# Optimization experiments

Hardware: AMD Instinct MI355X
Metric: run time of the kernel (lower is better)

Reference implementation:

```python
import jax, jax.numpy as jnp
import numpy as np

K = 16  # hardcoded in the torch module (reshape([-1, 16]))


def setup_inputs() -> dict:
    key = jax.random.key(0)
    B, M = 32, 2048
    N = B * M
    ks = jax.random.split(key, 7)
    pos = jax.random.normal(ks[0], (N, 3), dtype=jnp.float32)
    batch = jnp.repeat(jnp.arange(B, dtype=jnp.int32), M)  # sorted, equal-size graphs

    def lin(k_, fi, fo):
        lim = 1.0 / np.sqrt(fi)
        w = jax.random.uniform(k_, (fi, fo), jnp.float32, -lim, lim)
        b = jax.random.uniform(jax.random.fold_in(k_, 1), (fo,), jnp.float32, -lim, lim)
        return w, b

    W1, b1 = lin(ks[1], K * 6, 1024)
    W2, b2 = lin(ks[2], 1024, 256)
    W3, b3 = lin(ks[3], 256, 9)
    return {"pos": pos, "batch": batch, "num_graphs": B,
            "W1": W1, "b1": b1, "W2": W2, "b2": b2, "W3": W3, "b3": b3}


def _knn_idx(pos, num_graphs):
    # equal-size graphs laid out contiguously -> batched brute-force knn
    N = pos.shape[0]
    M = N // num_graphs
    p = pos.reshape(num_graphs, M, 3)
    sq = jnp.sum(p * p, axis=-1)                      # [B, M]
    # squared distances [B, M, M]; self-distance ~0 so loop=True self-edge is kept
    d2 = sq[:, :, None] + sq[:, None, :] - 2.0 * jnp.einsum('bid,bjd->bij', p, p)
    _, idx = jax.lax.top_k(-d2, K)                    # [B, M, K] local indices
    offs = (jnp.arange(num_graphs, dtype=idx.dtype) * M)[:, None, None]
    return (idx + offs).reshape(N, K)                 # global neighbour indices


def reference(pos, batch, num_graphs, W1, b1, W2, b2, W3, b3):
    N = pos.shape[0]
    M = N // num_graphs
    nbr_idx = _knn_idx(pos, num_graphs)               # [N, K]
    neighbours = pos[nbr_idx]                         # [N, K, 3] gather
    center = pos[:, None, :]                          # [N, 1, 3]
    feat = jnp.concatenate(
        [jnp.broadcast_to(center, (N, K, 3)), center - neighbours], axis=2
    ).reshape(N, K * 6)                               # [N, 96]
    h = jax.nn.relu(feat @ W1 + b1)
    h = jax.nn.relu(h @ W2 + b2)
    x9 = h @ W3 + b3                                  # [N, 9]
    pooled = x9.reshape(num_graphs, M, 9).mean(axis=1)  # global_mean_pool -> [B, 9]
    T = pooled[batch].reshape(N, 3, 3)                # gather back per node
    return jnp.einsum('nd,ndk->nk', pos, T)           # bmm([N,1,3],[N,3,3]) squeezed
```

## Files before the change

kernel.cpp:

```cpp
#include <hip/hip_runtime.h>
#include <stdint.h>

#define NPTS   65536
#define MPTS   2048
#define NGRAPH 32

typedef short s16x8 __attribute__((ext_vector_type(8)));
typedef float f32x4 __attribute__((ext_vector_type(4)));

#define FEATP_OFF 0u
#define W1P_OFF   12582912u
#define W2P_OFF   12779520u
#define SACC_OFF  13303808u
#define POOLT_OFF 13336576u

__device__ __forceinline__ unsigned short f2bf(float f) {
  unsigned u = __float_as_uint(f);
  u = (u + 0x7FFFu + ((u >> 16) & 1u)) >> 16;
  return (unsigned short)u;
}

__device__ __forceinline__ void ce32(unsigned& a, unsigned& b) {
  unsigned lo = __builtin_elementwise_min(a, b);
  b = __builtin_elementwise_max(a, b);
  a = lo;
}

template <int N>
__device__ __forceinline__ void sortN(unsigned* k) {
#pragma unroll
  for (int p = 1; p < N; p <<= 1)
#pragma unroll
    for (int q = p; q >= 1; q >>= 1)
#pragma unroll
      for (int j = q % p; j + q < N; j += 2 * q)
#pragma unroll
        for (int i = 0; i < q; ++i)
          if (i + j + q < N)
            if ((i + j) / (2 * p) == (i + j + q) / (2 * p))
              ce32(k[i + j], k[i + j + q]);
}

__device__ __forceinline__ void mergelow8(unsigned r[8], const unsigned b[8]) {
#pragma unroll
  for (int i = 0; i < 8; ++i)
    r[i] = __builtin_elementwise_min(r[i], b[7 - i]);
#pragma unroll
  for (int d = 4; d >= 1; d >>= 1)
#pragma unroll
    for (int i = 0; i < 8; ++i)
      if ((i & d) == 0) ce32(r[i], r[i + d]);
}

__device__ __forceinline__ void mergelow16(unsigned r[16], const unsigned b[16]) {
#pragma unroll
  for (int i = 0; i < 16; ++i)
    r[i] = __builtin_elementwise_min(r[i], b[15 - i]);
#pragma unroll
  for (int d = 8; d >= 1; d >>= 1)
#pragma unroll
    for (int i = 0; i < 16; ++i)
      if ((i & d) == 0) ce32(r[i], r[i + d]);
}

__global__ __launch_bounds__(256) void pack_w(
    const float* __restrict__ W1, const float* __restrict__ W2,
    unsigned short* __restrict__ w1p, unsigned short* __restrict__ w2p,
    float* __restrict__ sacc)
{
  int tid = blockIdx.x * 256 + threadIdx.x;
  if (tid < 96 * 1024) {
    int k = tid >> 10, n = tid & 1023;
    int kt = k >> 5, h = (k >> 3) & 3, j = k & 7;
    int nt = n >> 4, cc = n & 15;
    w1p[((size_t)(kt * 64 + nt) * 64 + h * 16 + cc) * 8 + j] = f2bf(W1[tid]);
  } else if (tid < 98304 + 262144) {
    int t = tid - 98304;
    int k = t >> 8, n = t & 255;
    int kt = k >> 5, h = (k >> 3) & 3, j = k & 7;
    int nt = n >> 4, cc = n & 15;
    w2p[((size_t)(kt * 16 + nt) * 64 + h * 16 + cc) * 8 + j] = f2bf(W2[t]);
  } else if (tid < 360448 + 8192) {
    sacc[tid - 360448] = 0.0f;
  }
}

__global__ __launch_bounds__(512, 4) void knn_feat(
    const float* __restrict__ pos, unsigned short* __restrict__ featp)
{
  __shared__ float4 pts[MPTS];
  int g = blockIdx.x >> 5;
  const float* gp = pos + (size_t)g * MPTS * 3;
  for (int i = threadIdx.x; i < MPTS; i += 512) {
    float x = gp[i * 3], y = gp[i * 3 + 1], z = gp[i * 3 + 2];
    float sq = fmaf(x, x, fmaf(y, y, z * z));
    pts[(i >> 8) + ((i & 255) << 3)] = make_float4(x, y, z, sq);
  }
  __syncthreads();

  int l = threadIdx.x & 63, w = threadIdx.x >> 6;
  int s = l >> 3, qlocal = l & 7;
  int ql = ((blockIdx.x & 31) << 6) + w * 8 + qlocal;
  float4 c = pts[(ql >> 8) + ((ql & 255) << 3)];
  float cs = c.w;
  unsigned sbase = (unsigned)(s << 8);

  unsigned run[8];

  {
    unsigned k[16];
#pragma unroll
    for (int t = 0; t < 16; ++t) {
      float4 p = pts[s + (t << 3)];
      float dot = fmaf(c.x, p.x, fmaf(c.y, p.y, c.z * p.z));
      float d2 = fmaf(-2.0f, dot, cs + p.w);
      k[t] = (__float_as_uint(d2) & 0xFFFFF800u) | sbase | (unsigned)t;
    }
    sortN<8>(k); sortN<8>(k + 8);
    mergelow8(k, k + 8);
#pragma unroll
    for (int i = 0; i < 8; ++i) run[i] = k[i];
  }
  for (int ch = 1; ch < 16; ++ch) {
    unsigned bch = sbase | (unsigned)(ch * 16);
    unsigned k[16];
#pragma unroll
    for (int t = 0; t < 16; ++t) {
      int i = ch * 16 + t;
      float4 p = pts[s + (i << 3)];
      float dot = fmaf(c.x, p.x, fmaf(c.y, p.y, c.z * p.z));
      float d2 = fmaf(-2.0f, dot, cs + p.w);
      k[t] = (__float_as_uint(d2) & 0xFFFFF800u) | bch | (unsigned)t;
    }
    sortN<8>(k); sortN<8>(k + 8);
    mergelow8(k, k + 8);
    mergelow8(run, k);
  }

  unsigned t16[16];
  {
    unsigned oth[8];
#pragma unroll
    for (int i = 0; i < 8; ++i) oth[i] = __shfl_xor(run[i], 8, 64);
#pragma unroll
    for (int i = 0; i < 8; ++i) {
      unsigned a = run[i], x = oth[7 - i];
      t16[i]     = __builtin_elementwise_min(a, x);
      t16[i + 8] = __builtin_elementwise_max(a, x);
    }
#pragma unroll
    for (int d = 4; d >= 1; d >>= 1)
#pragma unroll
      for (int i = 0; i < 16; ++i)
        if ((i & d) == 0) ce32(t16[i], t16[i + d]);
  }
#pragma unroll
  for (int m = 16; m <= 32; m <<= 1) {
    unsigned o2[16];
#pragma unroll
    for (int i = 0; i < 16; ++i) o2[i] = __shfl_xor(t16[i], m, 64);
    mergelow16(t16, o2);
  }

  if (s == 0) {
    float nx[16], ny[16], nz[16];
#pragma unroll
    for (int i = 0; i < 16; ++i) {
      int j = (int)(t16[i] & 0x7ffu);
      float4 p = pts[(j >> 8) + ((j & 255) << 3)];
      nx[i] = p.x; ny[i] = p.y; nz[i] = p.z;
    }
    int n = g * MPTS + ql;
    unsigned short* op = featp + (size_t)(n >> 4) * 1536 + (size_t)(n & 15) * 8;
#pragma unroll
    for (int kt = 0; kt < 3; ++kt) {
#pragma unroll
      for (int h = 0; h < 4; ++h) {
        s16x8 v;
#pragma unroll
        for (int j = 0; j < 8; ++j) {
          int f = kt * 32 + h * 8 + j;
          int kn = f / 6, comp = f % 6;
          float val;
          if      (comp == 0) val = c.x;
          else if (comp == 1) val = c.y;
          else if (comp == 2) val = c.z;
          else if (comp == 3) val = c.x - nx[kn];
          else if (comp == 4) val = c.y - ny[kn];
          else                val = c.z - nz[kn];
          v[j] = (short)f2bf(val);
        }
        *(s16x8*)(op + kt * 512 + h * 128) = v;
      }
    }
  }
}

__global__ __launch_bounds__(512, 2) void mlp_fused(
    const unsigned short* __restrict__ featp,
    const unsigned short* __restrict__ w1p,
    const unsigned short* __restrict__ w2p,
    const float* __restrict__ b1, const float* __restrict__ b2,
    float* __restrict__ sacc)
{
  __shared__ unsigned short h1c[2][64][136];

  int tid = threadIdx.x;
  int w = tid >> 6, lane = tid & 63;
  int b = blockIdx.x;
  int g = b >> 5;
  int ks = lane >> 4;
  int cl = lane & 15;

  s16x8 a1[4][3];
#pragma unroll
  for (int m = 0; m < 4; ++m) {
    const unsigned short* ap = featp + (size_t)(b * 4 + m) * 1536 + (size_t)lane * 8;
#pragma unroll
    for (int kt = 0; kt < 3; ++kt) a1[m][kt] = *(const s16x8*)(ap + kt * 512);
  }

  f32x4 acc2[4][2];
#pragma unroll
  for (int m = 0; m < 4; ++m) {
    acc2[m][0] = (f32x4){0, 0, 0, 0};
    acc2[m][1] = (f32x4){0, 0, 0, 0};
  }

  s16x8 b1f[3];
#pragma unroll
  for (int kt = 0; kt < 3; ++kt)
    b1f[kt] = *(const s16x8*)(w1p + ((size_t)(kt * 64 + w) * 64 + lane) * 8);

  for (int c = 0; c < 8; ++c) {
    int buf = c & 1;
    s16x8 b2f[8];
#pragma unroll
    for (int kt2 = 0; kt2 < 4; ++kt2)
#pragma unroll
      for (int j = 0; j < 2; ++j)
        b2f[kt2 * 2 + j] = *(const s16x8*)(
            w2p + ((size_t)((c * 4 + kt2) * 16 + (w * 2 + j)) * 64 + lane) * 8);

    float bias1 = b1[(c * 8 + w) * 16 + cl];
#pragma unroll
    for (int m = 0; m < 4; ++m) {
      f32x4 acc1 = (f32x4){0, 0, 0, 0};
#pragma unroll
      for (int kt = 0; kt < 3; ++kt)
        acc1 = __builtin_amdgcn_mfma_f32_16x16x32_bf16(a1[m][kt], b1f[kt], acc1, 0, 0, 0);
#pragma unroll
      for (int r = 0; r < 4; ++r) {
        float v = acc1[r] + bias1;
        v = v > 0.0f ? v : 0.0f;
        h1c[buf][m * 16 + ks * 4 + r][w * 16 + cl] = f2bf(v);
      }
    }

    if (c < 7) {
#pragma unroll
      for (int kt = 0; kt < 3; ++kt)
        b1f[kt] = *(const s16x8*)(
            w1p + ((size_t)(kt * 64 + (c + 1) * 8 + w) * 64 + lane) * 8);
    }
    __syncthreads();

#pragma unroll
    for (int kt2 = 0; kt2 < 4; ++kt2) {
      s16x8 afr[4];
#pragma unroll
      for (int m = 0; m < 4; ++m)
        afr[m] = *(const s16x8*)&h1c[buf][m * 16 + cl][kt2 * 32 + ks * 8];
#pragma unroll
      for (int j = 0; j < 2; ++j)
#pragma unroll
        for (int m = 0; m < 4; ++m)
          acc2[m][j] = __builtin_amdgcn_mfma_f32_16x16x32_bf16(
              afr[m], b2f[kt2 * 2 + j], acc2[m][j], 0, 0, 0);
    }
  }

  float sj0 = 0.0f, sj1 = 0.0f;
  {
    float bias20 = b2[(2 * w + 0) * 16 + cl];
    float bias21 = b2[(2 * w + 1) * 16 + cl];
#pragma unroll
    for (int m = 0; m < 4; ++m)
#pragma unroll
      for (int r = 0; r < 4; ++r) {
        float v0 = acc2[m][0][r] + bias20;
        float v1 = acc2[m][1][r] + bias21;
        sj0 += v0 > 0.0f ? v0 : 0.0f;
        sj1 += v1 > 0.0f ? v1 : 0.0f;
      }
  }
#pragma unroll
  for (int m = 16; m <= 32; m <<= 1) {
    sj0 += __shfl_xor(sj0, m, 64);
    sj1 += __shfl_xor(sj1, m, 64);
  }
  if (ks == 0) {
    atomicAdd(&sacc[g * 256 + (2 * w + 0) * 16 + cl], sj0);
    atomicAdd(&sacc[g * 256 + (2 * w + 1) * 16 + cl], sj1);
  }
}

__global__ __launch_bounds__(96) void pool_w3(
    const float* __restrict__ sacc, const float* __restrict__ W3,
    const float* __restrict__ b3, float* __restrict__ pooledT)
{
  int gid = blockIdx.x * 96 + threadIdx.x;
  if (gid >= NGRAPH * 9) return;
  int g = gid / 9, o = gid % 9;
  float acc = 0.0f;
  const float* sp = sacc + g * 256;
#pragma unroll 8
  for (int k = 0; k < 256; ++k) acc = fmaf(sp[k], W3[k * 9 + o], acc);
  pooledT[gid] = fmaf(acc, 1.0f / (float)MPTS, b3[o]);
}

__global__ __launch_bounds__(256) void finalize(
    const float* __restrict__ pos, const int* __restrict__ batch,
    const float* __restrict__ pooledT, float* __restrict__ out)
{
  int n = blockIdx.x * 256 + threadIdx.x;
  if (n >= NPTS) return;
  int bb = batch[n];
  float px = pos[n * 3], py = pos[n * 3 + 1], pz = pos[n * 3 + 2];
  const float* P = pooledT + bb * 9;
#pragma unroll
  for (int k2 = 0; k2 < 3; ++k2)
    out[n * 3 + k2] = fmaf(px, P[k2], fmaf(py, P[3 + k2], pz * P[6 + k2]));
}

extern "C" void kernel_launch(void* const* d_in, const int* in_sizes, int n_in,
                              void* d_out, int out_size, void* d_ws, size_t ws_size,
                              hipStream_t stream) {
  const float* pos  = (const float*)d_in[0];
  const int*   batch = (const int*)d_in[1];
  const float* W1 = (const float*)d_in[3];
  const float* b1 = (const float*)d_in[4];
  const float* W2 = (const float*)d_in[5];
  const float* b2 = (const float*)d_in[6];
  const float* W3 = (const float*)d_in[7];
  const float* b3 = (const float*)d_in[8];

  char* ws = (char*)d_ws;
  unsigned short* featp = (unsigned short*)(ws + FEATP_OFF);
  unsigned short* w1p   = (unsigned short*)(ws + W1P_OFF);
  unsigned short* w2p   = (unsigned short*)(ws + W2P_OFF);
  float*          sacc  = (float*)(ws + SACC_OFF);
  float*          pooledT = (float*)(ws + POOLT_OFF);
  float*          out = (float*)d_out;

  pack_w<<<dim3(1440), dim3(256), 0, stream>>>(W1, W2, w1p, w2p, sacc);
  knn_feat<<<dim3(1024), dim3(512), 0, stream>>>(pos, featp);
  mlp_fused<<<dim3(1024), dim3(512), 0, stream>>>(featp, w1p, w2p, b1, b2, sacc);
  pool_w3<<<dim3(3), dim3(96), 0, stream>>>(sacc, W3, b3, pooledT);
  finalize<<<dim3(256), dim3(256), 0, stream>>>(pos, batch, pooledT, out);
}
```

Measured before the change: 122.5 us.

## Replace brute-force kNN with z-sorted window search and early termination

Adds a per-graph bitonic sort of points by z-coordinate in the prep kernel, merged with the weight-packing kernel. The kNN kernel then walks outward from each query's rank in z order in 64-point chunks and stops once the z-gap squared exceeds the current 16th-best distance. This avoids scanning all 2048 candidates per query. It adds a sort pass and data-dependent, wave-divergent loop counts; with Gaussian data the pruning in 1D may be weak, and the threshold uses truncated keys, so there is some risk around ties and exactness.

Result: slower. 170.4 us (+39.1%).

```diff
diff --git a/kernel.cpp b/kernel.cpp
--- a/kernel.cpp
+++ b/kernel.cpp
@@ -13,6 +13,7 @@
 #define W2P_OFF   12779520u
 #define SACC_OFF  13303808u
 #define POOLT_OFF 13336576u
+#define ZKEY_OFF  13337728u
 
 __device__ __forceinline__ unsigned short f2bf(float f) {
   unsigned u = __float_as_uint(f);
@@ -63,85 +64,123 @@
       if ((i & d) == 0) ce32(r[i], r[i + d]);
 }
 
-__global__ __launch_bounds__(256) void pack_w(
-    const float* __restrict__ W1, const float* __restrict__ W2,
+__global__ __launch_bounds__(512) void prep(
+    const float* __restrict__ pos, const float* __restrict__ W1,
+    const float* __restrict__ W2, unsigned* __restrict__ zkeysG,
     unsigned short* __restrict__ w1p, unsigned short* __restrict__ w2p,
     float* __restrict__ sacc)
 {
-  int tid = blockIdx.x * 256 + threadIdx.x;
-  if (tid < 96 * 1024) {
-    int k = tid >> 10, n = tid & 1023;
-    int kt = k >> 5, h = (k >> 3) & 3, j = k & 7;
-    int nt = n >> 4, cc = n & 15;
-    w1p[((size_t)(kt * 64 + nt) * 64 + h * 16 + cc) * 8 + j] = f2bf(W1[tid]);
-  } else if (tid < 98304 + 262144) {
-    int t = tid - 98304;
-    int k = t >> 8, n = t & 255;
-    int kt = k >> 5, h = (k >> 3) & 3, j = k & 7;
-    int nt = n >> 4, cc = n & 15;
-    w2p[((size_t)(kt * 16 + nt) * 64 + h * 16 + cc) * 8 + j] = f2bf(W2[t]);
-  } else if (tid < 360448 + 8192) {
-    sacc[tid - 360448] = 0.0f;
+  __shared__ unsigned sk[MPTS];
+  int b = blockIdx.x;
+  if (b < NGRAPH) {
+    const float* gp = pos + (size_t)b * MPTS * 3;
+#pragma unroll
+    for (int e = 0; e < 4; ++e) {
+      int i = threadIdx.x + (e << 9);
+      float z = gp[i * 3 + 2];
+      unsigned u = __float_as_uint(z);
+      u ^= ((unsigned)(((int)u) >> 31)) | 0x80000000u;
+      sk[i] = (u & 0xFFFFF800u) | (unsigned)i;
+    }
+    for (int k2 = 2; k2 <= MPTS; k2 <<= 1)
+      for (int j = k2 >> 1; j > 0; j >>= 1) {
+        __syncthreads();
+#pragma unroll
+        for (int e = 0; e < 4; ++e) {
+          int i = threadIdx.x + (e << 9);
+          int ix = i ^ j;
+          if (ix > i) {
+            unsigned a = sk[i], bb = sk[ix];
+            bool up = ((i & k2) == 0);
+            if ((a > bb) == up) { sk[i] = bb; sk[ix] = a; }
+          }
+        }
+      }
+    __syncthreads();
+#pragma unroll
+    for (int e = 0; e < 4; ++e) {
+      int i = threadIdx.x + (e << 9);
+      zkeysG[(b << 11) + i] = sk[i];
+    }
+  } else {
+    int pid = (b - NGRAPH) * 512 + threadIdx.x;
+    if (pid < 98304) {
+      int k = pid >> 10, n = pid & 1023;
+      int kt = k >> 5, h = (k >> 3) & 3, j = k & 7;
+      int nt = n >> 4, cc = n & 15;
+      w1p[((size_t)(kt * 64 + nt) * 64 + h * 16 + cc) * 8 + j] = f2bf(W1[pid]);
+    } else if (pid < 98304 + 262144) {
+      int t = pid - 98304;
+      int k = t >> 8, n = t & 255;
+      int kt = k >> 5, h = (k >> 3) & 3, j = k & 7;
+      int nt = n >> 4, cc = n & 15;
+      w2p[((size_t)(kt * 16 + nt) * 64 + h * 16 + cc) * 8 + j] = f2bf(W2[t]);
+    } else if (pid < 360448 + 8192) {
+      sacc[pid - 360448] = 0.0f;
+    }
   }
 }
 
 __global__ __launch_bounds__(512, 4) void knn_feat(
-    const float* __restrict__ pos, unsigned short* __restrict__ featp)
+    const float* __restrict__ pos, const unsigned* __restrict__ zkeysG,
+    unsigned short* __restrict__ featp)
 {
-  __shared__ float4 pts[MPTS];
+  __shared__ float4 zpts[MPTS];
   int g = blockIdx.x >> 5;
   const float* gp = pos + (size_t)g * MPTS * 3;
   for (int i = threadIdx.x; i < MPTS; i += 512) {
-    float x = gp[i * 3], y = gp[i * 3 + 1], z = gp[i * 3 + 2];
-    float sq = fmaf(x, x, fmaf(y, y, z * z));
-    pts[(i >> 8) + ((i & 255) << 3)] = make_float4(x, y, z, sq);
+    int o = (int)(zkeysG[(g << 11) + i] & 0x7FFu);
+    float x = gp[o * 3], y = gp[o * 3 + 1], z = gp[o * 3 + 2];
+    zpts[i] = make_float4(x, y, z, fmaf(x, x, fmaf(y, y, z * z)));
   }
   __syncthreads();
 
   int l = threadIdx.x & 63, w = threadIdx.x >> 6;
-  int s = l >> 3, qlocal = l & 7;
-  int ql = ((blockIdx.x & 31) << 6) + w * 8 + qlocal;
-  float4 c = pts[(ql >> 8) + ((ql & 255) << 3)];
-  float cs = c.w;
-  unsigned sbase = (unsigned)(s << 8);
+  int t = l & 7, qv = l >> 3;
+  int R = ((blockIdx.x & 31) << 6) + w * 8 + qv;
+  float4 c = zpts[R];
+  float cs = c.w, cz = c.z;
 
   unsigned run[8];
-
-  {
-    unsigned k[16];
-#pragma unroll
-    for (int t = 0; t < 16; ++t) {
-      float4 p = pts[s + (t << 3)];
-      float dot = fmaf(c.x, p.x, fmaf(c.y, p.y, c.z * p.z));
-      float d2 = fmaf(-2.0f, dot, cs + p.w);
-      k[t] = (__float_as_uint(d2) & 0xFFFFF800u) | sbase | (unsigned)t;
-    }
-    sortN<8>(k); sortN<8>(k + 8);
-    mergelow8(k, k + 8);
-#pragma unroll
-    for (int i = 0; i < 8; ++i) run[i] = k[i];
-  }
-  for (int ch = 1; ch < 16; ++ch) {
-    unsigned bch = sbase | (unsigned)(ch * 16);
-    unsigned k[16];
-#pragma unroll
-    for (int t = 0; t < 16; ++t) {
-      int i = ch * 16 + t;
-      float4 p = pts[s + (i << 3)];
-      float dot = fmaf(c.x, p.x, fmaf(c.y, p.y, c.z * p.z));
-      float d2 = fmaf(-2.0f, dot, cs + p.w);
-      k[t] = (__float_as_uint(d2) & 0xFFFFF800u) | bch | (unsigned)t;
-    }
-    sortN<8>(k); sortN<8>(k + 8);
-    mergelow8(k, k + 8);
+#pragma unroll
+  for (int i = 0; i < 8; ++i) run[i] = 0xFFFFFFFFu;
+
+  int LO = R, HI = R;
+  for (int step = 0; step < 34; ++step) {
+    float dzl = (LO > 0)    ? (cz - zpts[LO - 1].z) : 1e30f;
+    float dzr = (HI < MPTS) ? (zpts[HI].z - cz)     : 1e30f;
+    bool goR = dzr <= dzl;
+    int base = goR ? HI : LO - 64;
+    if (goR) HI += 64; else LO -= 64;
+
+    unsigned k[8];
+#pragma unroll
+    for (int kk = 0; kk < 8; ++kk) {
+      int p = base + t + (kk << 3);
+      int pc = min(max(p, 0), MPTS - 1);
+      float4 P = zpts[pc];
+      float dot = fmaf(c.x, P.x, fmaf(c.y, P.y, c.z * P.z));
+      float d2 = fmaf(-2.0f, dot, cs + P.w);
+      unsigned key = (__float_as_uint(d2) & 0xFFFFF800u) | (unsigned)pc;
+      k[kk] = ((unsigned)p < (unsigned)MPTS) ? key : 0xFFFFFFFFu;
+    }
+    sortN<8>(k);
     mergelow8(run, k);
+
+    unsigned t0 = run[7] | 0x7FFu;
+    unsigned thr = (t0 > 0xFFFEFFFFu) ? 0xFFFFFFFFu : t0 + 0x10000u;
+    float dl = (LO > 0)    ? (cz - zpts[LO - 1].z) : 0.0f;
+    float dr = (HI < MPTS) ? (zpts[HI].z - cz)     : 0.0f;
+    bool doneL = (LO <= 0)    || ((__float_as_uint(dl * dl) & 0xFFFFF800u) > thr);
+    bool doneR = (HI >= MPTS) || ((__float_as_uint(dr * dr) & 0xFFFFF800u) > thr);
+    if (__all(doneL && doneR)) break;
   }
 
   unsigned t16[16];
   {
     unsigned oth[8];
 #pragma unroll
-    for (int i = 0; i < 8; ++i) oth[i] = __shfl_xor(run[i], 8, 64);
+    for (int i = 0; i < 8; ++i) oth[i] = __shfl_xor(run[i], 1, 64);
 #pragma unroll
     for (int i = 0; i < 8; ++i) {
       unsigned a = run[i], x = oth[7 - i];
@@ -155,22 +194,23 @@
         if ((i & d) == 0) ce32(t16[i], t16[i + d]);
   }
 #pragma unroll
-  for (int m = 16; m <= 32; m <<= 1) {
+  for (int m = 2; m <= 4; m <<= 1) {
     unsigned o2[16];
 #pragma unroll
     for (int i = 0; i < 16; ++i) o2[i] = __shfl_xor(t16[i], m, 64);
     mergelow16(t16, o2);
   }
 
-  if (s == 0) {
+  if (t == 0) {
     float nx[16], ny[16], nz[16];
 #pragma unroll
     for (int i = 0; i < 16; ++i) {
-      int j = (int)(t16[i] & 0x7ffu);
-      float4 p = pts[(j >> 8) + ((j & 255) << 3)];
+      int rk = (int)(t16[i] & 0x7FFu);
+      float4 p = zpts[rk];
       nx[i] = p.x; ny[i] = p.y; nz[i] = p.z;
     }
-    int n = g * MPTS + ql;
+    int oq = (int)(zkeysG[(g << 11) + R] & 0x7FFu);
+    int n = g * MPTS + oq;
     unsigned short* op = featp + (size_t)(n >> 4) * 1536 + (size_t)(n & 15) * 8;
 #pragma unroll
     for (int kt = 0; kt < 3; ++kt) {
@@ -351,10 +391,11 @@
   unsigned short* w2p   = (unsigned short*)(ws + W2P_OFF);
   float*          sacc  = (float*)(ws + SACC_OFF);
   float*          pooledT = (float*)(ws + POOLT_OFF);
+  unsigned*       zkeysG = (unsigned*)(ws + ZKEY_OFF);
   float*          out = (float*)d_out;
 
-  pack_w<<<dim3(1440), dim3(256), 0, stream>>>(W1, W2, w1p, w2p, sacc);
-  knn_feat<<<dim3(1024), dim3(512), 0, stream>>>(pos, featp);
+  prep<<<dim3(752), dim3(512), 0, stream>>>(pos, W1, W2, zkeysG, w1p, w2p, sacc);
+  knn_feat<<<dim3(1024), dim3(512), 0, stream>>>(pos, zkeysG, featp);
   mlp_fused<<<dim3(1024), dim3(512), 0, stream>>>(featp, w1p, w2p, b1, b2, sacc);
   pool_w3<<<dim3(3), dim3(96), 0, stream>>>(sacc, W3, b3, pooledT);
   finalize<<<dim3(256), dim3(256), 0, stream>>>(pos, batch, pooledT, out);
```
